# Performance work log

Hardware: AMD Instinct MI355X
Metric: run time of the kernel (lower is better)

Reference implementation:

```python
import jax, jax.numpy as jnp
import numpy as np

C = 1024
N_HEADS = 16
HEAD_DIM = C // N_HEADS
D_FF = 4 * C
EPS = 1e-5


def setup_inputs() -> dict:
    key = jax.random.key(0)
    ks = jax.random.split(key, 6)
    B, T = 4, 2048
    x = jax.random.normal(ks[0], (B, T, C), dtype=jnp.float32)
    w_qkv = jax.random.normal(ks[1], (C, 3 * C), dtype=jnp.float32) * (C ** -0.5)
    w_proj = jax.random.normal(ks[2], (C, C), dtype=jnp.float32) * (C ** -0.5)
    w1 = jax.random.normal(ks[3], (C, D_FF), dtype=jnp.float32) * (C ** -0.5)
    b1 = jnp.zeros((D_FF,), dtype=jnp.float32)
    w2 = jax.random.normal(ks[4], (D_FF, C), dtype=jnp.float32) * (D_FF ** -0.5)
    b2 = jnp.zeros((C,), dtype=jnp.float32)
    ln1_g = jnp.ones((C,), dtype=jnp.float32)
    ln1_b = jnp.zeros((C,), dtype=jnp.float32)
    ln2_g = jnp.ones((C,), dtype=jnp.float32)
    ln2_b = jnp.zeros((C,), dtype=jnp.float32)
    return {"x": x, "ln1_g": ln1_g, "ln1_b": ln1_b, "ln2_g": ln2_g,
            "ln2_b": ln2_b, "w_qkv": w_qkv, "w_proj": w_proj,
            "w1": w1, "b1": b1, "w2": w2, "b2": b2}


def _layernorm(x, g, b):
    mu = jnp.mean(x, axis=-1, keepdims=True)
    var = jnp.mean(jnp.square(x - mu), axis=-1, keepdims=True)
    return (x - mu) * jax.lax.rsqrt(var + EPS) * g + b


def _attention(x, w_qkv, w_proj):
    B, T, Cdim = x.shape
    qkv = x @ w_qkv                                   # [B,T,3C]
    q, k, v = jnp.split(qkv, 3, axis=-1)
    # [B,T,C] -> [B,H,T,D]
    def heads(t):
        return t.reshape(B, T, N_HEADS, HEAD_DIM).transpose(0, 2, 1, 3)
    q, k, v = heads(q), heads(k), heads(v)
    scale = HEAD_DIM ** -0.5
    scores = jnp.einsum('bhqd,bhkd->bhqk', q, k) * scale  # [B,H,T,T]
    attn = jax.nn.softmax(scores, axis=-1)
    out = jnp.einsum('bhqk,bhkd->bhqd', attn, v)          # [B,H,T,D]
    out = out.transpose(0, 2, 1, 3).reshape(B, T, Cdim)
    return out @ w_proj


def reference(x, ln1_g, ln1_b, ln2_g, ln2_b, w_qkv, w_proj, w1, b1, w2, b2):
    x = x + _attention(_layernorm(x, ln1_g, ln1_b), w_qkv, w_proj)
    h = _layernorm(x, ln2_g, ln2_b)
    # exact (erf) GELU matches torch.nn.GELU default
    h = jax.nn.gelu(h @ w1 + b1, approximate=False) @ w2 + b2
    return x + h
```

## Files before the change

kernel.cpp:

```cpp
#include <hip/hip_runtime.h>
#include <hip/hip_bf16.h>
#include <math.h>

typedef __attribute__((ext_vector_type(8))) short bf16x8;
typedef __attribute__((ext_vector_type(4))) float f32x4;
typedef unsigned short ushort_t;

__device__ __forceinline__ ushort_t f2bf(float f) {
    union { float f; unsigned u; } v; v.f = f;
    unsigned r = v.u + 0x7FFF + ((v.u >> 16) & 1);
    return (ushort_t)(r >> 16);
}

__device__ __forceinline__ unsigned pack2bf(float a, float b) {
    union { float f; unsigned u; } x, y; x.f = a; y.f = b;
    return __builtin_amdgcn_perm(y.u + 0x8000u, x.u + 0x8000u, 0x07060302u);
}

__device__ __forceinline__ unsigned cvtpk2bf(float a, float b) {
    unsigned r;
    asm("v_cvt_pk_bf16_f32 %0, %1, %2" : "=v"(r) : "v"(a), "v"(b));
    return r;
}

__device__ __forceinline__ void gl2lds(const void* g, void* l) {
    __builtin_amdgcn_global_load_lds(
        (const __attribute__((address_space(1))) void*)g,
        (__attribute__((address_space(3))) void*)l, 16, 0, 0);
}

__device__ __forceinline__ float fast_gelu(float tt) {
    float t2 = tt * tt;
    float arg = tt * fmaf(0.07135481283f, t2, 1.595769122f);
    float e = __builtin_amdgcn_exp2f(arg * -1.442695041f);
    return tt * __builtin_amdgcn_rcpf(1.0f + e);
}

__global__ __launch_bounds__(256)
void tcast_all(const float* __restrict__ wqkv, const float* __restrict__ wproj,
               const float* __restrict__ w1, const float* __restrict__ w2,
               ushort_t* __restrict__ wqkvT, ushort_t* __restrict__ wprojT,
               ushort_t* __restrict__ w1T, ushort_t* __restrict__ w2T,
               float qscale) {
    __shared__ float tile[32][33];
    int id = blockIdx.x;
    const float* in; ushort_t* out; int R, Cc, gx, scale_n;
    if (id < 3072)      { in = wqkv;  out = wqkvT;  R = 1024; Cc = 3072; gx = 96;  scale_n = 1024; }
    else if (id < 4096) { id -= 3072; in = wproj; out = wprojT; R = 1024; Cc = 1024; gx = 32; scale_n = 0; }
    else if (id < 8192) { id -= 4096; in = w1;    out = w1T;    R = 1024; Cc = 4096; gx = 128; scale_n = 0; }
    else                { id -= 8192; in = w2;    out = w2T;    R = 4096; Cc = 1024; gx = 32; scale_n = 0; }
    int bc = (id % gx) * 32, br = (id / gx) * 32;
    int tx = threadIdx.x, ty = threadIdx.y;
    #pragma unroll
    for (int i = 0; i < 32; i += 8)
        tile[ty + i][tx] = in[(size_t)(br + ty + i) * Cc + bc + tx];
    __syncthreads();
    #pragma unroll
    for (int i = 0; i < 32; i += 8) {
        int n = bc + ty + i;
        float v = tile[tx][ty + i];
        if (n < scale_n) v *= qscale;
        out[(size_t)n * R + br + tx] = f2bf(v);
    }
}

__global__ __launch_bounds__(256)
void ln_kernel(const float* __restrict__ x, const float* __restrict__ g,
               const float* __restrict__ b, ushort_t* __restrict__ out) {
    const int row = blockIdx.x;
    const int t = threadIdx.x;
    const float4 xv = ((const float4*)(x + (size_t)row * 1024))[t];
    float s  = xv.x + xv.y + xv.z + xv.w;
    float ss = xv.x*xv.x + xv.y*xv.y + xv.z*xv.z + xv.w*xv.w;
    #pragma unroll
    for (int off = 32; off > 0; off >>= 1) {
        s  += __shfl_xor(s, off);
        ss += __shfl_xor(ss, off);
    }
    __shared__ float red[8];
    int wave = t >> 6, lane = t & 63;
    if (lane == 0) { red[wave] = s; red[4 + wave] = ss; }
    __syncthreads();
    s  = red[0] + red[1] + red[2] + red[3];
    ss = red[4] + red[5] + red[6] + red[7];
    float mu  = s * (1.0f / 1024.0f);
    float var = ss * (1.0f / 1024.0f) - mu * mu;
    float rstd = rsqrtf(var + 1e-5f);
    float4 gv = ((const float4*)g)[t];
    float4 bv = ((const float4*)b)[t];
    ushort4 o;
    o.x = f2bf((xv.x - mu) * rstd * gv.x + bv.x);
    o.y = f2bf((xv.y - mu) * rstd * gv.y + bv.y);
    o.z = f2bf((xv.z - mu) * rstd * gv.z + bv.z);
    o.w = f2bf((xv.w - mu) * rstd * gv.w + bv.w);
    ((ushort4*)(out + (size_t)row * 1024))[t] = o;
}

template<int MODE, int K, int N>
__global__ __launch_bounds__(256)
void gemm_bt(const ushort_t* __restrict__ A, const ushort_t* __restrict__ Bt,
             void* __restrict__ Cout, const float* __restrict__ bias,
             const float* __restrict__ res, ushort_t* __restrict__ vTout) {
    constexpr int BK = 64;
    __shared__ __align__(16) ushort_t As[128 * 64];
    __shared__ __align__(16) ushort_t Bs[128 * 64];
    const int tid = threadIdx.x;
    const int wave = tid >> 6, lane = tid & 63;
    const int quad = lane >> 4, l16 = lane & 15;
    const int m0 = blockIdx.y * 128, n0 = blockIdx.x * 128;
    const int wm = (wave >> 1) * 64, wn = (wave & 1) * 64;

    const int r0 = tid >> 3, pc = tid & 7;
    const int lc = pc ^ (r0 & 7);
    const ushort_t* aSrc = A  + (size_t)(m0 + r0) * K + lc * 8;
    const ushort_t* bSrc = Bt + (size_t)(n0 + r0) * K + lc * 8;
    char* aDst = (char*)As + wave * 1024;
    char* bDst = (char*)Bs + wave * 1024;
    const int swz = l16 & 7;

    f32x4 acc[4][4] = {};

    for (int k0 = 0; k0 < K; k0 += BK) {
        __syncthreads();
        #pragma unroll
        for (int c = 0; c < 4; ++c) {
            gl2lds(aSrc + (size_t)c * 32 * K + k0, aDst + c * 4096);
            gl2lds(bSrc + (size_t)c * 32 * K + k0, bDst + c * 4096);
        }
        __syncthreads();
        #pragma unroll
        for (int ks = 0; ks < 2; ++ks) {
            const int cko = ((ks * 4 + quad) ^ swz) * 8;
            bf16x8 af[4], bfr[4];
            #pragma unroll
            for (int i = 0; i < 4; ++i)
                af[i] = *(const bf16x8*)(&As[(wm + i * 16 + l16) * 64 + cko]);
            #pragma unroll
            for (int j = 0; j < 4; ++j)
                bfr[j] = *(const bf16x8*)(&Bs[(wn + j * 16 + l16) * 64 + cko]);
            #pragma unroll
            for (int i = 0; i < 4; ++i)
                #pragma unroll
                for (int j = 0; j < 4; ++j)
                    acc[i][j] = __builtin_amdgcn_mfma_f32_16x16x32_bf16(
                        af[i], bfr[j], acc[i][j], 0, 0, 0);
        }
    }

    if constexpr (MODE == 0) {
        if (vTout && n0 >= 2048) {
            #pragma unroll
            for (int i = 0; i < 4; ++i) {
                int m = m0 + wm + i * 16 + quad * 4;
                int bb = m >> 11, t = m & 2047;
                #pragma unroll
                for (int j = 0; j < 4; ++j) {
                    int nn = n0 - 2048 + wn + j * 16 + l16;
                    int h = nn >> 6, d = nn & 63;
                    uint2 pk;
                    pk.x = pack2bf(acc[i][j][0], acc[i][j][1]);
                    pk.y = pack2bf(acc[i][j][2], acc[i][j][3]);
                    *(uint2*)(vTout + ((size_t)(bb * 16 + h) * 64 + d) * 2048 + t) = pk;
                }
            }
            return;
        }
    }
    float bj[4];
    if constexpr (MODE == 2 || MODE == 3) {
        #pragma unroll
        for (int j = 0; j < 4; ++j) bj[j] = bias[n0 + wn + j * 16 + l16];
    }
    #pragma unroll
    for (int i = 0; i < 4; ++i) {
        #pragma unroll
        for (int j = 0; j < 4; ++j) {
            #pragma unroll
            for (int r = 0; r < 4; ++r) {
                int m = m0 + wm + i * 16 + quad * 4 + r;
                int n = n0 + wn + j * 16 + l16;
                size_t idx = (size_t)m * N + n;
                float v = acc[i][j][r];
                if constexpr (MODE == 0) {
                    ((ushort_t*)Cout)[idx] = f2bf(v);
                } else if constexpr (MODE == 1) {
                    ((float*)Cout)[idx] = v + res[idx];
                } else if constexpr (MODE == 2) {
                    ((ushort_t*)Cout)[idx] = f2bf(fast_gelu(v + bj[j]));
                } else {
                    ((float*)Cout)[idx] = v + bj[j] + res[idx];
                }
            }
        }
    }
}

__global__ __launch_bounds__(256)
void attn_kernel(const ushort_t* __restrict__ qkv, const ushort_t* __restrict__ vT,
                 ushort_t* __restrict__ out) {
    constexpr int T = 2048, C3 = 3072, BQ = 128;
    __shared__ __align__(16) ushort_t Ks[2][64 * 64];
    __shared__ __align__(16) ushort_t Vs[2][64 * 64];
    const int bh = blockIdx.x, b = bh >> 4, h = bh & 15;
    const int qt = blockIdx.y;
    const int tid = threadIdx.x, wave = tid >> 6, lane = tid & 63;
    const int quad = lane >> 4, l16 = lane & 15;
    const int swz = l16 & 7;

    bf16x8 qf[2][2];
    {
        const ushort_t* Qg = qkv + ((size_t)b * T + qt * BQ + wave * 32) * C3 + h * 64;
        #pragma unroll
        for (int i = 0; i < 2; ++i)
            #pragma unroll
            for (int ks = 0; ks < 2; ++ks)
                qf[i][ks] = *(const bf16x8*)(Qg + (size_t)(i * 16 + l16) * C3 + ks * 32 + quad * 8);
    }
    bf16x8 onesf;
    #pragma unroll
    for (int e = 0; e < 8; ++e) onesf[e] = (short)0x3F80;

    const int r0 = tid >> 3, pc = tid & 7;
    const int lc = pc ^ (r0 & 7);
    const ushort_t* KgB = qkv + (size_t)b * T * C3 + 1024 + h * 64 + (size_t)r0 * C3 + lc * 8;
    const ushort_t* VgB = vT + (size_t)bh * 64 * T + (size_t)r0 * T + lc * 8;
    char* kDst0 = (char*)&Ks[0][0] + wave * 1024;
    char* vDst0 = (char*)&Vs[0][0] + wave * 1024;

    f32x4 o_acc[2][4] = {};
    f32x4 l_acc[2] = {};

    #pragma unroll
    for (int c = 0; c < 2; ++c) {
        gl2lds(KgB + (size_t)c * 32 * C3, kDst0 + c * 4096);
        gl2lds(VgB + (size_t)c * 32 * T,  vDst0 + c * 4096);
    }

    for (int kt = 0; kt < T / 64; ++kt) {
        const int cur = kt & 1;
        __syncthreads();
        if (kt + 1 < T / 64) {
            const int nb = (cur ^ 1) * 8192;
            #pragma unroll
            for (int c = 0; c < 2; ++c) {
                gl2lds(KgB + ((size_t)(kt + 1) * 64 + c * 32) * C3, kDst0 + nb + c * 4096);
                gl2lds(VgB + (size_t)c * 32 * T + (kt + 1) * 64,    vDst0 + nb + c * 4096);
            }
        }
        const ushort_t* Kc = &Ks[cur][0];
        const ushort_t* Vc = &Vs[cur][0];

        f32x4 s[2][4] = {};
        #pragma unroll
        for (int ks = 0; ks < 2; ++ks) {
            const int cko = ((ks * 4 + quad) ^ swz) * 8;
            bf16x8 kf[4];
            #pragma unroll
            for (int j = 0; j < 4; ++j)
                kf[j] = *(const bf16x8*)(&Kc[(j * 16 + l16) * 64 + cko]);
            #pragma unroll
            for (int i = 0; i < 2; ++i)
                #pragma unroll
                for (int j = 0; j < 4; ++j)
                    s[i][j] = __builtin_amdgcn_mfma_f32_16x16x32_bf16(
                        kf[j], qf[i][ks], s[i][j], 0, 0, 0);
        }

        bf16x8 pf[2][2];
        #pragma unroll
        for (int i = 0; i < 2; ++i) {
            unsigned u[4][2];
            #pragma unroll
            for (int j = 0; j < 4; ++j) {
                float p0 = __builtin_amdgcn_exp2f(s[i][j][0]);
                float p1 = __builtin_amdgcn_exp2f(s[i][j][1]);
                float p2 = __builtin_amdgcn_exp2f(s[i][j][2]);
                float p3 = __builtin_amdgcn_exp2f(s[i][j][3]);
                u[j][0] = cvtpk2bf(p0, p1);
                u[j][1] = cvtpk2bf(p2, p3);
            }
            #pragma unroll
            for (int ks2 = 0; ks2 < 2; ++ks2) {
                unsigned d0 = u[2 * ks2][0], d2 = u[2 * ks2 + 1][0];
                asm("v_permlane32_swap_b32 %0, %1\n\t"
                    "v_permlane16_swap_b32 %0, %1" : "+v"(d0), "+v"(d2));
                unsigned d1 = u[2 * ks2][1], d3 = u[2 * ks2 + 1][1];
                asm("v_permlane32_swap_b32 %0, %1\n\t"
                    "v_permlane16_swap_b32 %0, %1" : "+v"(d1), "+v"(d3));
                union { unsigned d[4]; bf16x8 v; } fr;
                fr.d[0] = d0; fr.d[1] = d1; fr.d[2] = d2; fr.d[3] = d3;
                pf[i][ks2] = fr.v;
            }
        }

        #pragma unroll
        for (int ks2 = 0; ks2 < 2; ++ks2) {
            const int cko = ((ks2 * 4 + quad) ^ swz) * 8;
            bf16x8 vf[4];
            #pragma unroll
            for (int j = 0; j < 4; ++j)
                vf[j] = *(const bf16x8*)(&Vc[(j * 16 + l16) * 64 + cko]);
            #pragma unroll
            for (int i = 0; i < 2; ++i) {
                #pragma unroll
                for (int j = 0; j < 4; ++j)
                    o_acc[i][j] = __builtin_amdgcn_mfma_f32_16x16x32_bf16(
                        pf[i][ks2], vf[j], o_acc[i][j], 0, 0, 0);
                l_acc[i] = __builtin_amdgcn_mfma_f32_16x16x32_bf16(
                    pf[i][ks2], onesf, l_acc[i], 0, 0, 0);
            }
        }
    }

    #pragma unroll
    for (int i = 0; i < 2; ++i) {
        #pragma unroll
        for (int r = 0; r < 4; ++r) {
            float inv = 1.0f / l_acc[i][r];
            int row = qt * BQ + wave * 32 + i * 16 + quad * 4 + r;
            size_t orow = ((size_t)b * T + row) * 1024 + h * 64;
            #pragma unroll
            for (int j = 0; j < 4; ++j)
                out[orow + j * 16 + l16] = f2bf(o_acc[i][j][r] * inv);
        }
    }
}

extern "C" void kernel_launch(void* const* d_in, const int* in_sizes, int n_in,
                              void* d_out, int out_size, void* d_ws, size_t ws_size,
                              hipStream_t stream) {
    const float* x     = (const float*)d_in[0];
    const float* ln1g  = (const float*)d_in[1];
    const float* ln1b  = (const float*)d_in[2];
    const float* ln2g  = (const float*)d_in[3];
    const float* ln2b  = (const float*)d_in[4];
    const float* wqkv  = (const float*)d_in[5];
    const float* wproj = (const float*)d_in[6];
    const float* w1    = (const float*)d_in[7];
    const float* b1    = (const float*)d_in[8];
    const float* w2    = (const float*)d_in[9];
    const float* b2    = (const float*)d_in[10];
    float* out = (float*)d_out;

    const size_t MT = 8192;
    ushort_t* wqkvT  = (ushort_t*)d_ws;
    ushort_t* wprojT = wqkvT  + (size_t)3072 * 1024;
    ushort_t* w1T    = wprojT + (size_t)1024 * 1024;
    ushort_t* w2T    = w1T    + (size_t)4096 * 1024;
    ushort_t* xn     = w2T    + (size_t)1024 * 4096;
    ushort_t* qkvb   = xn     + MT * 1024;
    ushort_t* attnb  = qkvb   + MT * 3072;
    float*    x2     = (float*)(attnb + MT * 1024);
    ushort_t* xn2    = (ushort_t*)(x2 + MT * 1024);
    ushort_t* h1     = xn;
    ushort_t* vT     = (ushort_t*)x2;

    dim3 blk256(256);
    dim3 tblk(32, 8);
    const float qscale = 0.125f * 1.4426950408889634f;

    tcast_all<<<dim3(12288), tblk, 0, stream>>>(wqkv, wproj, w1, w2,
                                                wqkvT, wprojT, w1T, w2T, qscale);

    ln_kernel<<<dim3(8192), blk256, 0, stream>>>(x, ln1g, ln1b, xn);
    gemm_bt<0, 1024, 3072><<<dim3(24, 64), blk256, 0, stream>>>(xn, wqkvT, qkvb, nullptr, nullptr, vT);
    attn_kernel<<<dim3(64, 16), blk256, 0, stream>>>(qkvb, vT, attnb);
    gemm_bt<1, 1024, 1024><<<dim3(8, 64), blk256, 0, stream>>>(attnb, wprojT, x2, nullptr, x, nullptr);
    ln_kernel<<<dim3(8192), blk256, 0, stream>>>(x2, ln2g, ln2b, xn2);
    gemm_bt<2, 1024, 4096><<<dim3(32, 64), blk256, 0, stream>>>(xn2, w1T, h1, b1, nullptr, nullptr);
    gemm_bt<3, 4096, 1024><<<dim3(8, 64), blk256, 0, stream>>>(h1, w2T, out, b2, x2, nullptr);
}
```

Baseline: 493.1 us.

## Add 256x256 ping-pong pipelined GEMM for QKV and FFN-up projections

Introduces a new 512-thread GEMM kernel with 256x256 output tiles, double-buffered direct global-to-LDS loads interleaved with MFMA phases, setprio scheduling and a grouped workgroup-id remap for L2 locality. It replaces the 128-tile GEMM for the QKV projection (including the transposed-V epilogue) and the first FFN matmul with GELU. The goal is more operand reuse per tile and overlap of loads with matrix math. The cost is higher register and LDS use per block and fewer workgroups, which can hurt occupancy and tail balance.

```diff
diff --git a/kernel.cpp b/kernel.cpp
--- a/kernel.cpp
+++ b/kernel.cpp
@@ -147,25 +147,6 @@
         }
     }
 
-    if constexpr (MODE == 0) {
-        if (vTout && n0 >= 2048) {
-            #pragma unroll
-            for (int i = 0; i < 4; ++i) {
-                int m = m0 + wm + i * 16 + quad * 4;
-                int bb = m >> 11, t = m & 2047;
-                #pragma unroll
-                for (int j = 0; j < 4; ++j) {
-                    int nn = n0 - 2048 + wn + j * 16 + l16;
-                    int h = nn >> 6, d = nn & 63;
-                    uint2 pk;
-                    pk.x = pack2bf(acc[i][j][0], acc[i][j][1]);
-                    pk.y = pack2bf(acc[i][j][2], acc[i][j][3]);
-                    *(uint2*)(vTout + ((size_t)(bb * 16 + h) * 64 + d) * 2048 + t) = pk;
-                }
-            }
-            return;
-        }
-    }
     float bj[4];
     if constexpr (MODE == 2 || MODE == 3) {
         #pragma unroll
@@ -189,6 +170,148 @@
                     ((ushort_t*)Cout)[idx] = f2bf(fast_gelu(v + bj[j]));
                 } else {
                     ((float*)Cout)[idx] = v + bj[j] + res[idx];
+                }
+            }
+        }
+    }
+}
+
+template<int MODE, int K, int N>
+__global__ __launch_bounds__(512, 2)
+void gemm256p(const ushort_t* __restrict__ A, const ushort_t* __restrict__ Bt,
+              void* __restrict__ Cout, const float* __restrict__ bias,
+              const float* __restrict__ res, ushort_t* __restrict__ vTout) {
+    constexpr int BK = 64;
+    constexpr int NT = K / BK;
+    constexpr int ITERS = NT / 2;
+    __shared__ __align__(16) ushort_t As[2][256 * 64];
+    __shared__ __align__(16) ushort_t Bs[2][256 * 64];
+    const int tid = threadIdx.x;
+    const int wave = tid >> 6, lane = tid & 63;
+    const int quad = lane >> 4, l16 = lane & 15;
+    const int nwg = gridDim.x * gridDim.y;
+    int id = blockIdx.y * gridDim.x + blockIdx.x;
+    id = (id & 7) * (nwg >> 3) + (id >> 3);
+    const int m0 = (id / gridDim.x) * 256, n0 = (id % gridDim.x) * 256;
+    const int wm = (wave >> 2) * 128, wn = (wave & 3) * 64;
+    const int r0 = tid >> 3, pc = tid & 7;
+    const int lc = pc ^ (r0 & 7);
+    const ushort_t* aSrc = A  + (size_t)(m0 + r0) * K + lc * 8;
+    const ushort_t* bSrc = Bt + (size_t)(n0 + r0) * K + lc * 8;
+    const int swz = l16 & 7;
+
+    f32x4 acc[8][4] = {};
+    bf16x8 bfr[4][2], af[2][2];
+
+    #define STA(t, b, c) gl2lds(aSrc + (size_t)(t) * BK + (size_t)(c) * 64 * K, \
+                                (char*)&As[b][0] + (c) * 8192 + wave * 1024)
+    #define STB(t, b, c) gl2lds(bSrc + (size_t)(t) * BK + (size_t)(c) * 64 * K, \
+                                (char*)&Bs[b][0] + (c) * 8192 + wave * 1024)
+    #define LDB(buf) { _Pragma("unroll") for (int j = 0; j < 4; ++j) \
+        _Pragma("unroll") for (int ks = 0; ks < 2; ++ks) \
+            bfr[j][ks] = *(const bf16x8*)(&Bs[buf][(wn + j * 16 + l16) * 64 + ((ks * 4 + quad) ^ swz) * 8]); }
+    #define LDA2(buf, fb) { _Pragma("unroll") for (int f = 0; f < 2; ++f) \
+        _Pragma("unroll") for (int ks = 0; ks < 2; ++ks) \
+            af[f][ks] = *(const bf16x8*)(&As[buf][(wm + ((fb) + f) * 16 + l16) * 64 + ((ks * 4 + quad) ^ swz) * 8]); }
+    #define BARW { __builtin_amdgcn_s_barrier(); \
+        asm volatile("s_waitcnt lgkmcnt(0)" ::: "memory"); \
+        __builtin_amdgcn_sched_barrier(0); }
+    #define MM(fb) { __builtin_amdgcn_s_setprio(1); \
+        _Pragma("unroll") for (int ks = 0; ks < 2; ++ks) \
+        _Pragma("unroll") for (int f = 0; f < 2; ++f) \
+        _Pragma("unroll") for (int j = 0; j < 4; ++j) \
+            acc[(fb) + f][j] = __builtin_amdgcn_mfma_f32_16x16x32_bf16( \
+                af[f][ks], bfr[j][ks], acc[(fb) + f][j], 0, 0, 0); \
+        __builtin_amdgcn_s_setprio(0); }
+    #define CBAR __builtin_amdgcn_s_barrier();
+
+    STB(0, 0, 0); STB(0, 0, 1); STB(0, 0, 2); STB(0, 0, 3);
+    STA(0, 0, 0); STA(0, 0, 1); STA(0, 0, 2); STA(0, 0, 3);
+    STB(1, 1, 0); STB(1, 1, 1); STB(1, 1, 2); STB(1, 1, 3);
+    asm volatile("s_waitcnt vmcnt(4)" ::: "memory");
+    __builtin_amdgcn_s_barrier();
+
+    for (int i = 0; i < ITERS; ++i) {
+        const int e = 2 * i, o = 2 * i + 1;
+        const bool pre = (i + 1 < ITERS);
+        LDB(0); LDA2(0, 0);
+        STA(o, 1, 0); STA(o, 1, 1);
+        BARW; MM(0); CBAR;
+        LDA2(0, 2);
+        STA(o, 1, 2); STA(o, 1, 3);
+        if (pre) { STB(e + 2, 0, 0); STB(e + 2, 0, 1); }
+        BARW; MM(2); CBAR;
+        LDA2(0, 4);
+        if (pre) { STB(e + 2, 0, 2); STB(e + 2, 0, 3); }
+        BARW; MM(4); CBAR;
+        LDA2(0, 6);
+        BARW; MM(6);
+        if (pre) asm volatile("s_waitcnt vmcnt(4)" ::: "memory");
+        else     asm volatile("s_waitcnt vmcnt(0)" ::: "memory");
+        CBAR;
+        LDB(1); LDA2(1, 0);
+        if (pre) { STA(e + 2, 0, 0); STA(e + 2, 0, 1); }
+        BARW; MM(0); CBAR;
+        LDA2(1, 2);
+        if (pre) { STA(e + 2, 0, 2); STA(e + 2, 0, 3); }
+        BARW; MM(2); CBAR;
+        LDA2(1, 4);
+        if (pre) { STB(o + 2, 1, 0); STB(o + 2, 1, 1); }
+        BARW; MM(4); CBAR;
+        LDA2(1, 6);
+        if (pre) { STB(o + 2, 1, 2); STB(o + 2, 1, 3); }
+        BARW; MM(6);
+        if (pre) {
+            asm volatile("s_waitcnt vmcnt(4)" ::: "memory");
+            CBAR;
+        }
+    }
+    #undef STA
+    #undef STB
+    #undef LDB
+    #undef LDA2
+    #undef BARW
+    #undef MM
+    #undef CBAR
+
+    if constexpr (MODE == 0) {
+        if (vTout && n0 >= 2048) {
+            #pragma unroll
+            for (int i = 0; i < 8; ++i) {
+                int m = m0 + wm + i * 16 + quad * 4;
+                int bb = m >> 11, tq = m & 2047;
+                #pragma unroll
+                for (int j = 0; j < 4; ++j) {
+                    int nn = n0 - 2048 + wn + j * 16 + l16;
+                    int h = nn >> 6, d = nn & 63;
+                    uint2 pk;
+                    pk.x = pack2bf(acc[i][j][0], acc[i][j][1]);
+                    pk.y = pack2bf(acc[i][j][2], acc[i][j][3]);
+                    *(uint2*)(vTout + ((size_t)(bb * 16 + h) * 64 + d) * 2048 + tq) = pk;
+                }
+            }
+            return;
+        }
+    }
+    float bj[4];
+    if constexpr (MODE == 2) {
+        #pragma unroll
+        for (int j = 0; j < 4; ++j) bj[j] = bias[n0 + wn + j * 16 + l16];
+    }
+    #pragma unroll
+    for (int i = 0; i < 8; ++i) {
+        #pragma unroll
+        for (int j = 0; j < 4; ++j) {
+            #pragma unroll
+            for (int r = 0; r < 4; ++r) {
+                int m = m0 + wm + i * 16 + quad * 4 + r;
+                int n = n0 + wn + j * 16 + l16;
+                size_t idx = (size_t)m * N + n;
+                float v = acc[i][j][r];
+                if constexpr (MODE == 0) {
+                    ((ushort_t*)Cout)[idx] = f2bf(v);
+                } else if constexpr (MODE == 2) {
+                    ((ushort_t*)Cout)[idx] = f2bf(fast_gelu(v + bj[j]));
                 }
             }
         }
@@ -356,6 +479,7 @@
     ushort_t* vT     = (ushort_t*)x2;
 
     dim3 blk256(256);
+    dim3 blk512(512);
     dim3 tblk(32, 8);
     const float qscale = 0.125f * 1.4426950408889634f;
 
@@ -363,10 +487,10 @@
                                                 wqkvT, wprojT, w1T, w2T, qscale);
 
     ln_kernel<<<dim3(8192), blk256, 0, stream>>>(x, ln1g, ln1b, xn);
-    gemm_bt<0, 1024, 3072><<<dim3(24, 64), blk256, 0, stream>>>(xn, wqkvT, qkvb, nullptr, nullptr, vT);
+    gemm256p<0, 1024, 3072><<<dim3(12, 32), blk512, 0, stream>>>(xn, wqkvT, qkvb, nullptr, nullptr, vT);
     attn_kernel<<<dim3(64, 16), blk256, 0, stream>>>(qkvb, vT, attnb);
     gemm_bt<1, 1024, 1024><<<dim3(8, 64), blk256, 0, stream>>>(attnb, wprojT, x2, nullptr, x, nullptr);
     ln_kernel<<<dim3(8192), blk256, 0, stream>>>(x2, ln2g, ln2b, xn2);
-    gemm_bt<2, 1024, 4096><<<dim3(32, 64), blk256, 0, stream>>>(xn2, w1T, h1, b1, nullptr, nullptr);
+    gemm256p<2, 1024, 4096><<<dim3(16, 32), blk512, 0, stream>>>(xn2, w1T, h1, b1, nullptr, nullptr);
     gemm_bt<3, 4096, 1024><<<dim3(8, 64), blk256, 0, stream>>>(h1, w2T, out, b2, x2, nullptr);
 }
```

Result: no change. 495.1 us (+0.4%).
